# Kernel optimization log

Hardware: AMD Instinct MI355X
Metric: run time of the kernel (lower is better)

## Reference

```python
import jax, jax.numpy as jnp
import numpy as np

L, B, H, HC = 2048, 64, 1024, 1024
NEG = -1e10


def setup_inputs() -> dict:
    key = jax.random.key(0)
    k1, k2, k3, k4, k5, k6 = jax.random.split(key, 6)
    prev_layer_outputs = jax.random.normal(k1, (L, B, H), dtype=jnp.float32)
    hidden = jax.random.normal(k2, (B, H), dtype=jnp.float32)
    mask = jax.random.randint(k3, (B, L), 0, 2, dtype=jnp.int32)
    # learned params: e = Linear(2H -> HC), v = Linear(HC -> 1, no bias)
    s_e = 1.0 / np.sqrt(2 * H)
    W_e = jax.random.uniform(k4, (HC, 2 * H), minval=-s_e, maxval=s_e, dtype=jnp.float32)
    b_e = jax.random.uniform(k5, (HC,), minval=-s_e, maxval=s_e, dtype=jnp.float32)
    s_v = 1.0 / np.sqrt(HC)
    W_v = jax.random.uniform(k6, (HC,), minval=-s_v, maxval=s_v, dtype=jnp.float32)
    return {"prev_layer_outputs": prev_layer_outputs, "hidden": hidden, "mask": mask,
            "W_e": W_e, "b_e": b_e, "W_v": W_v}


def reference(prev_layer_outputs, hidden, mask, W_e, b_e, W_v):
    # prev_layer_outputs: [L, B, H] -> [B, L, H]
    outs = jnp.transpose(prev_layer_outputs, (1, 0, 2))
    # repeat hidden over L and concat on feature dim: [B, L, 2H]
    hid = jnp.broadcast_to(hidden[:, None, :], (outs.shape[0], outs.shape[1], hidden.shape[-1]))
    cat = jnp.concatenate([hid, outs], axis=-1)
    # energy: tanh(Linear(2H -> HC))
    energy = jnp.tanh(jnp.einsum('blf,cf->blc', cat, W_e) + b_e)
    # score: Linear(HC -> 1), squeeze -> [B, L]
    attention = jnp.einsum('blc,c->bl', energy, W_v)
    attention = jnp.where(mask == 0, jnp.float32(NEG), attention)
    attention_weights = jax.nn.softmax(attention, axis=1)  # [B, L]
    # weighted sum over L -> [B, H], then to [1, B, H]
    weighted = jnp.einsum('bl,blh->bh', attention_weights, outs)
    return weighted[None, :, :]
```

## Files before the change

### kernel.cpp

```cpp
#include <hip/hip_runtime.h>
#include <hip/hip_bf16.h>
#include <stdint.h>

#define LDIM 2048
#define BDIM 64
#define HDIM 1024
#define HCDIM 1024
#define CAPROWS 98304

typedef __attribute__((ext_vector_type(8))) short short8;
typedef __attribute__((ext_vector_type(4))) short s16x4;
typedef __attribute__((ext_vector_type(4))) float f32x4;

static __device__ __forceinline__ short f2bf(float f) {
  union { float f; uint32_t u; } a; a.f = f;
  uint32_t r = a.u + 0x7fffu + ((a.u >> 16) & 1u);
  return (short)(r >> 16);
}
static __device__ __forceinline__ float bf2f(short s) {
  union { uint32_t u; float f; } a;
  a.u = ((uint32_t)(unsigned short)s) << 16;
  return a.f;
}
static __device__ __forceinline__ float fast_tanh(float x) {
  x = fminf(15.f, fmaxf(-15.f, x));
  float e = __expf(2.f * x);
  return (e - 1.f) * __builtin_amdgcn_rcpf(e + 1.f);
}

#define GL16(gp, lp) __builtin_amdgcn_global_load_lds(                           \
    (const __attribute__((address_space(1))) void*)(gp),                         \
    (__attribute__((address_space(3))) void*)(lp), 16, 0, 0)

__global__ void scan_mask(const int* __restrict__ mask, int* __restrict__ bases) {
  __shared__ int sc[512];
  const int t = threadIdx.x;
  int cnt = 0;
  #pragma unroll 8
  for (int b = 0; b < 64; ++b) {
    int4 v = *(const int4*)&mask[b * 2048 + t * 4];
    cnt += v.x + v.y + v.z + v.w;
  }
  sc[t] = cnt;
  __syncthreads();
  for (int off = 1; off < 512; off <<= 1) {
    int v = (t >= off) ? sc[t - off] : 0;
    __syncthreads();
    sc[t] += v;
    __syncthreads();
  }
  bases[t] = sc[t] - cnt;
  if (t == 511) bases[512] = sc[511];
}

__global__ void gather_rows(const float* __restrict__ prev, const int* __restrict__ mask,
                            const int* __restrict__ bases, short* __restrict__ A_c,
                            int* __restrict__ cm2m, int* __restrict__ m2cm) {
  __shared__ int smm[256];
  __shared__ int swt[4];
  const int c = blockIdx.x, t = threadIdx.x;
  const int base = bases[c];
  int bit = 0, p = 0, wv = 0;
  if (t < 256) {
    const int m = c * 256 + t;
    bit = (mask[(t & 63) * 2048 + (m >> 6)] != 0);
    unsigned long long bal = __ballot(bit);
    const int lane = t & 63;
    wv = t >> 6;
    p = __popcll(bal & ((1ull << lane) - 1ull));
    if (lane == 0) swt[wv] = (int)__popcll(bal);
  }
  __syncthreads();
  if (t < 256 && bit) {
    int off = p;
    for (int i = 0; i < wv; ++i) off += swt[i];
    const int cm = base + off;
    smm[off] = t;
    if (cm < CAPROWS) {
      cm2m[cm] = c * 256 + t;
      m2cm[c * 256 + t] = cm;
    }
  }
  __syncthreads();
  const int cnt = swt[0] + swt[1] + swt[2] + swt[3];
  const int col = (t & 255) * 4;
  for (int r = (t >> 8); r < cnt; r += 2) {
    const int lm = smm[r];
    const float4 v = *(const float4*)(prev + (((size_t)(c * 256 + lm)) << 10) + col);
    if (base + r < CAPROWS) {
      s16x4 o = { f2bf(v.x), f2bf(v.y), f2bf(v.z), f2bf(v.w) };
      *(s16x4*)&A_c[(((size_t)(base + r)) << 10) + col] = o;
    }
  }
}

__global__ void convert_we(const float* __restrict__ We, short* __restrict__ Wb) {
  int g = blockIdx.x * 256 + threadIdx.x;
  int c = g >> 8;
  int j = (g & 255) * 4;
  float4 v = *(const float4*)(We + (size_t)c * 2048 + 1024 + j);
  s16x4 o = { f2bf(v.x), f2bf(v.y), f2bf(v.z), f2bf(v.w) };
  *(s16x4*)(Wb + (size_t)c * 1024 + j) = o;
}

__global__ void hidbias_kernel(const float* __restrict__ We, const float* __restrict__ hidden,
                               const float* __restrict__ be, float* __restrict__ hidbias) {
  __shared__ float wrow[1024];
  int c0 = blockIdx.x * 16;
  int t = threadIdx.x;
  int b = t >> 2, q = t & 3;
  for (int ci = 0; ci < 16; ++ci) {
    int c = c0 + ci;
    *(float4*)&wrow[t * 4] = *(const float4*)&We[(size_t)c * 2048 + t * 4];
    __syncthreads();
    float s0 = 0.f, s1 = 0.f;
    const float* hb = hidden + b * 1024;
    #pragma unroll 8
    for (int j = 0; j < 256; j += 2) {
      int i0 = q + 4 * j;
      s0 += wrow[i0] * hb[i0];
      s1 += wrow[i0 + 4] * hb[i0 + 4];
    }
    float s = s0 + s1;
    s += __shfl_xor(s, 1);
    s += __shfl_xor(s, 2);
    if (q == 0) hidbias[b * 1024 + c] = s + be[c];
    __syncthreads();
  }
}

__global__ __launch_bounds__(512) void energy_gemm_p6(
    const short* __restrict__ A_c, const short* __restrict__ Wb,
    const float* __restrict__ hidbias, const float* __restrict__ Wv,
    const int* __restrict__ bases, const int* __restrict__ cm2m,
    float* __restrict__ logitsT)
{
  __shared__ short As[4][256][32];
  __shared__ short Bs[4][256][32];
  __shared__ int sidx[256];
  const int Mc0 = bases[512];
  const int Mc = Mc0 < CAPROWS ? Mc0 : CAPROWS;
  const int mt = ((blockIdx.x >> 5) << 3) + (blockIdx.x & 7);
  const int nt = (blockIdx.x >> 3) & 3;
  if (mt * 256 >= Mc) return;
  const int m0 = mt * 256;
  const int n0 = nt * 256;

  const int tid = threadIdx.x;
  const int wave = tid >> 6, lane = tid & 63;
  const int q = lane >> 4, lr = lane & 15;
  const int wr = wave >> 2, wc = wave & 3;

  const int r0 = tid >> 2;
  const int c0s = (((tid & 3) ^ ((r0 >> 1) & 3))) * 8;
  const short* asrc = A_c + (size_t)(m0 + r0) * 1024 + c0s;
  const short* bsrc = Wb  + (size_t)(n0 + r0) * 1024 + c0s;

#define STAGE(buf, ks) do {                                                    \
    const int _ko = (ks) * 32;                                                 \
    GL16(asrc + _ko,          &As[buf][0][0] + tid * 8);                       \
    GL16(asrc + 131072 + _ko, &As[buf][0][0] + tid * 8 + 4096);                \
    GL16(bsrc + _ko,          &Bs[buf][0][0] + tid * 8);                       \
    GL16(bsrc + 131072 + _ko, &Bs[buf][0][0] + tid * 8 + 4096);                \
  } while (0)

  const int crd = (q ^ ((lr >> 1) & 3)) * 8;

#define COMPUTE(buf) do {                                                      \
    short8 af[8], bfr[4];                                                      \
    _Pragma("unroll")                                                          \
    for (int mi = 0; mi < 8; ++mi)                                             \
      af[mi] = *(const short8*)&As[buf][wr * 128 + mi * 16 + lr][crd];         \
    _Pragma("unroll")                                                          \
    for (int ni = 0; ni < 4; ++ni)                                             \
      bfr[ni] = *(const short8*)&Bs[buf][wc * 64 + ni * 16 + lr][crd];         \
    __builtin_amdgcn_s_setprio(1);                                             \
    _Pragma("unroll")                                                          \
    for (int mi = 0; mi < 8; ++mi)                                             \
      _Pragma("unroll")                                                        \
      for (int ni = 0; ni < 4; ++ni)                                           \
        acc[mi][ni] = __builtin_amdgcn_mfma_f32_16x16x32_bf16(                 \
            af[mi], bfr[ni], acc[mi][ni], 0, 0, 0);                            \
    __builtin_amdgcn_s_setprio(0);                                             \
  } while (0)

#define VMW8() asm volatile("s_waitcnt vmcnt(8)" ::: "memory")
#define VMW4() asm volatile("s_waitcnt vmcnt(4)" ::: "memory")
#define VMW0() asm volatile("s_waitcnt vmcnt(0)" ::: "memory")
#define BAR()  asm volatile("s_barrier" ::: "memory")

  f32x4 acc[8][4];
  #pragma unroll
  for (int i = 0; i < 8; ++i)
    #pragma unroll
    for (int j = 0; j < 4; ++j) acc[i][j] = (f32x4){0.f, 0.f, 0.f, 0.f};

  STAGE(0, 0);
  STAGE(1, 1);
  STAGE(2, 2);

  #pragma unroll 4
  for (int ks = 0; ks < 28; ++ks) {
    VMW8(); BAR();
    STAGE((ks + 3) & 3, ks + 3);
    COMPUTE(ks & 3);
  }
  VMW8(); BAR(); STAGE(3, 31); COMPUTE(0);
  VMW8(); BAR(); COMPUTE(1);
  VMW4(); BAR(); COMPUTE(2);
  VMW0(); BAR(); COMPUTE(3);

#undef STAGE
#undef COMPUTE

  if (tid < 256) sidx[tid] = (m0 + tid < Mc) ? cm2m[m0 + tid] : -1;
  __syncthreads();

  float wv[4];
  #pragma unroll
  for (int ni = 0; ni < 4; ++ni) wv[ni] = Wv[n0 + wc * 64 + ni * 16 + lr];

  #pragma unroll
  for (int mi = 0; mi < 8; ++mi) {
    #pragma unroll
    for (int r = 0; r < 4; ++r) {
      const int row = wr * 128 + mi * 16 + 4 * q + r;
      const int mm = sidx[row];
      if (mm >= 0) {
        const int b = mm & 63;
        float s = 0.f;
        #pragma unroll
        for (int ni = 0; ni < 4; ++ni) {
          const int c = n0 + wc * 64 + ni * 16 + lr;
          s += fast_tanh(acc[mi][ni][r] + hidbias[b * 1024 + c]) * wv[ni];
        }
        s += __shfl_xor(s, 1);
        s += __shfl_xor(s, 2);
        s += __shfl_xor(s, 4);
        s += __shfl_xor(s, 8);
        if (lr == 0) atomicAdd(&logitsT[mm], s);
      }
    }
  }
}

__global__ void softstats(const float* __restrict__ logitsT, const int* __restrict__ mask,
                          float* __restrict__ stats) {
  __shared__ float red[8];
  const int b = blockIdx.x, t = threadIdx.x;
  float mx = -1e30f;
  for (int l = t; l < 2048; l += 256)
    if (mask[b * 2048 + l] != 0) mx = fmaxf(mx, logitsT[l * 64 + b]);
  #pragma unroll
  for (int o = 32; o > 0; o >>= 1) mx = fmaxf(mx, __shfl_xor(mx, o));
  if ((t & 63) == 0) red[t >> 6] = mx;
  __syncthreads();
  mx = fmaxf(fmaxf(red[0], red[1]), fmaxf(red[2], red[3]));
  float den = 0.f;
  for (int l = t; l < 2048; l += 256)
    if (mask[b * 2048 + l] != 0) den += __expf(logitsT[l * 64 + b] - mx);
  #pragma unroll
  for (int o = 32; o > 0; o >>= 1) den += __shfl_xor(den, o);
  if ((t & 63) == 0) red[4 + (t >> 6)] = den;
  __syncthreads();
  if (t == 0) {
    stats[b * 2] = mx;
    stats[b * 2 + 1] = 1.f / (red[4] + red[5] + red[6] + red[7]);
  }
}

__global__ void wsum_bf16(const short* __restrict__ A_c, const float* __restrict__ logitsT,
                          const int* __restrict__ mask, const float* __restrict__ stats,
                          const int* __restrict__ m2cm, float* __restrict__ out) {
  const int b = blockIdx.x >> 5;
  const int lc = blockIdx.x & 31;
  const int t = threadIdx.x;
  const float mx = stats[b * 2], invd = stats[b * 2 + 1];
  const int h0 = t * 4;
  float4 a = {0.f, 0.f, 0.f, 0.f};
  for (int l = lc * 64; l < lc * 64 + 64; ++l) {
    if (mask[b * 2048 + l] == 0) continue;
    const unsigned cm = (unsigned)m2cm[l * 64 + b];
    if (cm >= (unsigned)CAPROWS) continue;
    float w = __expf(logitsT[l * 64 + b] - mx) * invd;
    s16x4 v = *(const s16x4*)&A_c[((size_t)cm << 10) + h0];
    a.x += w * bf2f(v.x);
    a.y += w * bf2f(v.y);
    a.z += w * bf2f(v.z);
    a.w += w * bf2f(v.w);
  }
  atomicAdd(&out[b * 1024 + h0 + 0], a.x);
  atomicAdd(&out[b * 1024 + h0 + 1], a.y);
  atomicAdd(&out[b * 1024 + h0 + 2], a.z);
  atomicAdd(&out[b * 1024 + h0 + 3], a.w);
}

extern "C" void kernel_launch(void* const* d_in, const int* in_sizes, int n_in,
                              void* d_out, int out_size, void* d_ws, size_t ws_size,
                              hipStream_t stream) {
  const float* prev   = (const float*)d_in[0];
  const float* hidden = (const float*)d_in[1];
  const int*   mask   = (const int*)d_in[2];
  const float* We     = (const float*)d_in[3];
  const float* be     = (const float*)d_in[4];
  const float* Wv     = (const float*)d_in[5];
  float* out = (float*)d_out;

  char* ws = (char*)d_ws;
  size_t off = 0;
  short* A_c     = (short*)(ws + off); off += (size_t)CAPROWS * 1024 * 2;
  short* Wb      = (short*)(ws + off); off += 2097152;
  float* hidbias = (float*)(ws + off); off += 262144;
  float* logitsT = (float*)(ws + off); off += 524288;
  int*   cm2m    = (int*)  (ws + off); off += (size_t)CAPROWS * 4;
  int*   m2cm    = (int*)  (ws + off); off += 524288;
  int*   bases   = (int*)  (ws + off); off += 4096;
  float* stats   = (float*)(ws + off); off += 1024;

  hipMemsetAsync(d_out, 0, (size_t)out_size * sizeof(float), stream);
  hipMemsetAsync(logitsT, 0, 131072 * sizeof(float), stream);
  scan_mask<<<1, 512, 0, stream>>>(mask, bases);
  gather_rows<<<512, 512, 0, stream>>>(prev, mask, bases, A_c, cm2m, m2cm);
  convert_we<<<1024, 256, 0, stream>>>(We, Wb);
  hidbias_kernel<<<64, 256, 0, stream>>>(We, hidden, be, hidbias);
  energy_gemm_p6<<<2048, 512, 0, stream>>>(A_c, Wb, hidbias, Wv, bases, cm2m, logitsT);
  softstats<<<64, 256, 0, stream>>>(logitsT, mask, stats);
  wsum_bf16<<<2048, 256, 0, stream>>>(A_c, logitsT, mask, stats, m2cm, out);
}
```

Measured before the change: 468.1 us.

## Restructure energy GEMM into 8-phase ping-pong pipeline with 64-wide K tiles

Replaces the 4-buffer, K=32 staging loop with a double-buffered K=64 scheme split into A/B halves. Each K-step is broken into four phases that interleave global-to-LDS loads of the next tile with LDS reads and MFMA batches. Barriers sit between phases and the LDS swizzle changes to an XOR over 8 chunks. The goal is to hide load latency behind matrix math with fewer wait points and bigger tiles. In exchange it adds many more barriers per step, and the last iteration reloads a redundant tile.

```diff
diff --git a/kernel.cpp b/kernel.cpp
--- a/kernel.cpp
+++ b/kernel.cpp
@@ -129,14 +129,14 @@
   }
 }
 
-__global__ __launch_bounds__(512) void energy_gemm_p6(
+__global__ __launch_bounds__(512) void energy_gemm_8p(
     const short* __restrict__ A_c, const short* __restrict__ Wb,
     const float* __restrict__ hidbias, const float* __restrict__ Wv,
     const int* __restrict__ bases, const int* __restrict__ cm2m,
     float* __restrict__ logitsT)
 {
-  __shared__ short As[4][256][32];
-  __shared__ short Bs[4][256][32];
+  __shared__ short Ah[2][2][128][64];
+  __shared__ short Bh[2][2][128][64];
   __shared__ int sidx[256];
   const int Mc0 = bases[512];
   const int Mc = Mc0 < CAPROWS ? Mc0 : CAPROWS;
@@ -150,44 +150,50 @@
   const int wave = tid >> 6, lane = tid & 63;
   const int q = lane >> 4, lr = lane & 15;
   const int wr = wave >> 2, wc = wave & 3;
-
-  const int r0 = tid >> 2;
-  const int c0s = (((tid & 3) ^ ((r0 >> 1) & 3))) * 8;
-  const short* asrc = A_c + (size_t)(m0 + r0) * 1024 + c0s;
-  const short* bsrc = Wb  + (size_t)(n0 + r0) * 1024 + c0s;
-
-#define STAGE(buf, ks) do {                                                    \
-    const int _ko = (ks) * 32;                                                 \
-    GL16(asrc + _ko,          &As[buf][0][0] + tid * 8);                       \
-    GL16(asrc + 131072 + _ko, &As[buf][0][0] + tid * 8 + 4096);                \
-    GL16(bsrc + _ko,          &Bs[buf][0][0] + tid * 8);                       \
-    GL16(bsrc + 131072 + _ko, &Bs[buf][0][0] + tid * 8 + 4096);                \
-  } while (0)
-
-  const int crd = (q ^ ((lr >> 1) & 3)) * 8;
-
-#define COMPUTE(buf) do {                                                      \
-    short8 af[8], bfr[4];                                                      \
+  const int bh = wc >> 1;
+
+  const int sr  = tid >> 3;
+  const int sck = ((tid & 7) ^ ((tid >> 3) & 7)) * 8;
+
+#define STAGE_A(buf, h, kt) do {                                               \
+    const short* _s = A_c + (size_t)(m0 + (h) * 128 + sr) * 1024 + (kt) * 64 + sck; \
+    GL16(_s,         &Ah[buf][h][0][0] + tid * 8);                             \
+    GL16(_s + 65536, &Ah[buf][h][0][0] + tid * 8 + 4096);                      \
+  } while (0)
+#define STAGE_B(buf, h, kt) do {                                               \
+    const short* _s = Wb + (size_t)(n0 + (h) * 128 + sr) * 1024 + (kt) * 64 + sck; \
+    GL16(_s,         &Bh[buf][h][0][0] + tid * 8);                             \
+    GL16(_s + 65536, &Bh[buf][h][0][0] + tid * 8 + 4096);                      \
+  } while (0)
+
+#define DSREAD_A(buf, kk) do {                                                 \
     _Pragma("unroll")                                                          \
     for (int mi = 0; mi < 8; ++mi)                                             \
-      af[mi] = *(const short8*)&As[buf][wr * 128 + mi * 16 + lr][crd];         \
+      afA[mi] = *(const short8*)&Ah[buf][wr][mi * 16 + lr]                     \
+                    [((((kk) * 4 + q)) ^ (lr & 7)) * 8];                       \
+  } while (0)
+#define DSREAD_B(dst, buf, kk, p) do {                                         \
     _Pragma("unroll")                                                          \
-    for (int ni = 0; ni < 4; ++ni)                                             \
-      bfr[ni] = *(const short8*)&Bs[buf][wc * 64 + ni * 16 + lr][crd];         \
+    for (int j = 0; j < 2; ++j)                                                \
+      dst[j] = *(const short8*)&Bh[buf][bh][(wc & 1) * 64 + ((p) * 2 + j) * 16 + lr] \
+                   [((((kk) * 4 + q)) ^ (lr & 7)) * 8];                        \
+  } while (0)
+
+#define MM(p, bf) do {                                                         \
     __builtin_amdgcn_s_setprio(1);                                             \
     _Pragma("unroll")                                                          \
-    for (int mi = 0; mi < 8; ++mi)                                             \
-      _Pragma("unroll")                                                        \
-      for (int ni = 0; ni < 4; ++ni)                                           \
-        acc[mi][ni] = __builtin_amdgcn_mfma_f32_16x16x32_bf16(                 \
-            af[mi], bfr[ni], acc[mi][ni], 0, 0, 0);                            \
+    for (int mi = 0; mi < 8; ++mi) {                                           \
+      acc[mi][(p) * 2]     = __builtin_amdgcn_mfma_f32_16x16x32_bf16(          \
+          afA[mi], bf[0], acc[mi][(p) * 2], 0, 0, 0);                          \
+      acc[mi][(p) * 2 + 1] = __builtin_amdgcn_mfma_f32_16x16x32_bf16(          \
+          afA[mi], bf[1], acc[mi][(p) * 2 + 1], 0, 0, 0);                      \
+    }                                                                          \
     __builtin_amdgcn_s_setprio(0);                                             \
   } while (0)
 
-#define VMW8() asm volatile("s_waitcnt vmcnt(8)" ::: "memory")
-#define VMW4() asm volatile("s_waitcnt vmcnt(4)" ::: "memory")
-#define VMW0() asm volatile("s_waitcnt vmcnt(0)" ::: "memory")
-#define BAR()  asm volatile("s_barrier" ::: "memory")
+#define VM2()  asm volatile("s_waitcnt vmcnt(2)" ::: "memory")
+#define LGKM() asm volatile("s_waitcnt lgkmcnt(0)" ::: "memory")
+#define BARR() asm volatile("s_barrier" ::: "memory")
 
   f32x4 acc[8][4];
   #pragma unroll
@@ -195,23 +201,34 @@
     #pragma unroll
     for (int j = 0; j < 4; ++j) acc[i][j] = (f32x4){0.f, 0.f, 0.f, 0.f};
 
-  STAGE(0, 0);
-  STAGE(1, 1);
-  STAGE(2, 2);
-
-  #pragma unroll 4
-  for (int ks = 0; ks < 28; ++ks) {
-    VMW8(); BAR();
-    STAGE((ks + 3) & 3, ks + 3);
-    COMPUTE(ks & 3);
-  }
-  VMW8(); BAR(); STAGE(3, 31); COMPUTE(0);
-  VMW8(); BAR(); COMPUTE(1);
-  VMW4(); BAR(); COMPUTE(2);
-  VMW0(); BAR(); COMPUTE(3);
-
-#undef STAGE
-#undef COMPUTE
+  short8 afA[8], bfrA[2], bfrB[2];
+
+  STAGE_A(0, 0, 0); STAGE_B(0, 0, 0); STAGE_A(0, 1, 0); STAGE_B(0, 1, 0);
+
+  for (int ks = 0; ks < 16; ++ks) {
+    const int cb = ks & 1, nb = cb ^ 1;
+    const int nx = (ks < 15) ? ks + 1 : 15;
+    STAGE_A(nb, 0, nx);
+    VM2(); BARR();
+    DSREAD_A(cb, 0); DSREAD_B(bfrA, cb, 0, 0);
+    LGKM(); MM(0, bfrA); BARR();
+    DSREAD_B(bfrB, cb, 0, 1);
+    STAGE_B(nb, 0, nx);
+    BARR(); LGKM(); MM(1, bfrB); BARR();
+    DSREAD_A(cb, 1); DSREAD_B(bfrA, cb, 1, 0);
+    STAGE_A(nb, 1, nx);
+    BARR(); LGKM(); MM(0, bfrA); BARR();
+    DSREAD_B(bfrB, cb, 1, 1);
+    STAGE_B(nb, 1, nx);
+    BARR(); LGKM(); MM(1, bfrB); BARR();
+  }
+  asm volatile("s_waitcnt vmcnt(0)" ::: "memory");
+
+#undef STAGE_A
+#undef STAGE_B
+#undef DSREAD_A
+#undef DSREAD_B
+#undef MM
 
   if (tid < 256) sidx[tid] = (m0 + tid < Mc) ? cm2m[m0 + tid] : -1;
   __syncthreads();
@@ -323,7 +340,7 @@
   gather_rows<<<512, 512, 0, stream>>>(prev, mask, bases, A_c, cm2m, m2cm);
   convert_we<<<1024, 256, 0, stream>>>(We, Wb);
   hidbias_kernel<<<64, 256, 0, stream>>>(We, hidden, be, hidbias);
-  energy_gemm_p6<<<2048, 512, 0, stream>>>(A_c, Wb, hidbias, Wv, bases, cm2m, logitsT);
+  energy_gemm_8p<<<2048, 512, 0, stream>>>(A_c, Wb, hidbias, Wv, bases, cm2m, logitsT);
   softstats<<<64, 256, 0, stream>>>(logitsT, mask, stats);
   wsum_bf16<<<2048, 256, 0, stream>>>(A_c, logitsT, mask, stats, m2cm, out);
 }
```

Measured after the change: 489.1 us. +4.5%, slower.

## Replace mask scan with atomic row allocation and shrink GEMM tiles to 128

Applied to the files above, without the earlier changes.

Drops the single-block scan_mask kernel and has each gather block claim its compacted output range with an atomicAdd on a global counter. This removes a serial launch, and the row order now depends on atomic scheduling. The energy GEMM moves from 256x256 tiles with 512 threads to 128x128 tiles with 256 threads and two blocks per CU. The aim is to cut wasted work on the partial last tile and to raise occupancy, at the cost of less operand reuse per tile and more redundant loads.

```diff
diff --git a/kernel.cpp b/kernel.cpp
--- a/kernel.cpp
+++ b/kernel.cpp
@@ -32,34 +32,13 @@
     (const __attribute__((address_space(1))) void*)(gp),                         \
     (__attribute__((address_space(3))) void*)(lp), 16, 0, 0)
 
-__global__ void scan_mask(const int* __restrict__ mask, int* __restrict__ bases) {
-  __shared__ int sc[512];
-  const int t = threadIdx.x;
-  int cnt = 0;
-  #pragma unroll 8
-  for (int b = 0; b < 64; ++b) {
-    int4 v = *(const int4*)&mask[b * 2048 + t * 4];
-    cnt += v.x + v.y + v.z + v.w;
-  }
-  sc[t] = cnt;
-  __syncthreads();
-  for (int off = 1; off < 512; off <<= 1) {
-    int v = (t >= off) ? sc[t - off] : 0;
-    __syncthreads();
-    sc[t] += v;
-    __syncthreads();
-  }
-  bases[t] = sc[t] - cnt;
-  if (t == 511) bases[512] = sc[511];
-}
-
 __global__ void gather_rows(const float* __restrict__ prev, const int* __restrict__ mask,
-                            const int* __restrict__ bases, short* __restrict__ A_c,
+                            int* __restrict__ counter, short* __restrict__ A_c,
                             int* __restrict__ cm2m, int* __restrict__ m2cm) {
   __shared__ int smm[256];
   __shared__ int swt[4];
+  __shared__ int sbase;
   const int c = blockIdx.x, t = threadIdx.x;
-  const int base = bases[c];
   int bit = 0, p = 0, wv = 0;
   if (t < 256) {
     const int m = c * 256 + t;
@@ -71,6 +50,10 @@
     if (lane == 0) swt[wv] = (int)__popcll(bal);
   }
   __syncthreads();
+  const int cnt = swt[0] + swt[1] + swt[2] + swt[3];
+  if (t == 0) sbase = atomicAdd(counter, cnt);
+  __syncthreads();
+  const int base = sbase;
   if (t < 256 && bit) {
     int off = p;
     for (int i = 0; i < wv; ++i) off += swt[i];
@@ -82,7 +65,6 @@
     }
   }
   __syncthreads();
-  const int cnt = swt[0] + swt[1] + swt[2] + swt[3];
   const int col = (t & 255) * 4;
   for (int r = (t >> 8); r < cnt; r += 2) {
     const int lm = smm[r];
@@ -129,27 +111,27 @@
   }
 }
 
-__global__ __launch_bounds__(512) void energy_gemm_p6(
+__global__ __launch_bounds__(256, 2) void energy_gemm_128p(
     const short* __restrict__ A_c, const short* __restrict__ Wb,
     const float* __restrict__ hidbias, const float* __restrict__ Wv,
-    const int* __restrict__ bases, const int* __restrict__ cm2m,
+    const int* __restrict__ counter, const int* __restrict__ cm2m,
     float* __restrict__ logitsT)
 {
-  __shared__ short As[4][256][32];
-  __shared__ short Bs[4][256][32];
-  __shared__ int sidx[256];
-  const int Mc0 = bases[512];
+  __shared__ short As[4][128][32];
+  __shared__ short Bs[4][128][32];
+  __shared__ int sidx[128];
+  const int Mc0 = counter[0];
   const int Mc = Mc0 < CAPROWS ? Mc0 : CAPROWS;
-  const int mt = ((blockIdx.x >> 5) << 3) + (blockIdx.x & 7);
-  const int nt = (blockIdx.x >> 3) & 3;
-  if (mt * 256 >= Mc) return;
-  const int m0 = mt * 256;
-  const int n0 = nt * 256;
+  const int mt = ((blockIdx.x >> 6) << 3) + (blockIdx.x & 7);
+  const int nt = (blockIdx.x >> 3) & 7;
+  if (mt * 128 >= Mc) return;
+  const int m0 = mt * 128;
+  const int n0 = nt * 128;
 
   const int tid = threadIdx.x;
   const int wave = tid >> 6, lane = tid & 63;
   const int q = lane >> 4, lr = lane & 15;
-  const int wr = wave >> 2, wc = wave & 3;
+  const int wr = wave >> 1, wc = wave & 1;
 
   const int r0 = tid >> 2;
   const int c0s = (((tid & 3) ^ ((r0 >> 1) & 3))) * 8;
@@ -158,25 +140,25 @@
 
 #define STAGE(buf, ks) do {                                                    \
     const int _ko = (ks) * 32;                                                 \
-    GL16(asrc + _ko,          &As[buf][0][0] + tid * 8);                       \
-    GL16(asrc + 131072 + _ko, &As[buf][0][0] + tid * 8 + 4096);                \
-    GL16(bsrc + _ko,          &Bs[buf][0][0] + tid * 8);                       \
-    GL16(bsrc + 131072 + _ko, &Bs[buf][0][0] + tid * 8 + 4096);                \
+    GL16(asrc + _ko,         &As[buf][0][0] + tid * 8);                        \
+    GL16(asrc + 65536 + _ko, &As[buf][0][0] + tid * 8 + 2048);                 \
+    GL16(bsrc + _ko,         &Bs[buf][0][0] + tid * 8);                        \
+    GL16(bsrc + 65536 + _ko, &Bs[buf][0][0] + tid * 8 + 2048);                 \
   } while (0)
 
   const int crd = (q ^ ((lr >> 1) & 3)) * 8;
 
 #define COMPUTE(buf) do {                                                      \
-    short8 af[8], bfr[4];                                                      \
+    short8 af[4], bfr[4];                                                      \
     _Pragma("unroll")                                                          \
-    for (int mi = 0; mi < 8; ++mi)                                             \
-      af[mi] = *(const short8*)&As[buf][wr * 128 + mi * 16 + lr][crd];         \
+    for (int mi = 0; mi < 4; ++mi)                                             \
+      af[mi] = *(const short8*)&As[buf][wr * 64 + mi * 16 + lr][crd];          \
     _Pragma("unroll")                                                          \
     for (int ni = 0; ni < 4; ++ni)                                             \
       bfr[ni] = *(const short8*)&Bs[buf][wc * 64 + ni * 16 + lr][crd];         \
     __builtin_amdgcn_s_setprio(1);                                             \
     _Pragma("unroll")                                                          \
-    for (int mi = 0; mi < 8; ++mi)                                             \
+    for (int mi = 0; mi < 4; ++mi)                                             \
       _Pragma("unroll")                                                        \
       for (int ni = 0; ni < 4; ++ni)                                           \
         acc[mi][ni] = __builtin_amdgcn_mfma_f32_16x16x32_bf16(                 \
@@ -189,9 +171,9 @@
 #define VMW0() asm volatile("s_waitcnt vmcnt(0)" ::: "memory")
 #define BAR()  asm volatile("s_barrier" ::: "memory")
 
-  f32x4 acc[8][4];
-  #pragma unroll
-  for (int i = 0; i < 8; ++i)
+  f32x4 acc[4][4];
+  #pragma unroll
+  for (int i = 0; i < 4; ++i)
     #pragma unroll
     for (int j = 0; j < 4; ++j) acc[i][j] = (f32x4){0.f, 0.f, 0.f, 0.f};
 
@@ -213,7 +195,7 @@
 #undef STAGE
 #undef COMPUTE
 
-  if (tid < 256) sidx[tid] = (m0 + tid < Mc) ? cm2m[m0 + tid] : -1;
+  if (tid < 128) sidx[tid] = (m0 + tid < Mc) ? cm2m[m0 + tid] : -1;
   __syncthreads();
 
   float wv[4];
@@ -221,10 +203,10 @@
   for (int ni = 0; ni < 4; ++ni) wv[ni] = Wv[n0 + wc * 64 + ni * 16 + lr];
 
   #pragma unroll
-  for (int mi = 0; mi < 8; ++mi) {
+  for (int mi = 0; mi < 4; ++mi) {
     #pragma unroll
     for (int r = 0; r < 4; ++r) {
-      const int row = wr * 128 + mi * 16 + 4 * q + r;
+      const int row = wr * 64 + mi * 16 + 4 * q + r;
       const int mm = sidx[row];
       if (mm >= 0) {
         const int b = mm & 63;
@@ -312,18 +294,17 @@
   short* Wb      = (short*)(ws + off); off += 2097152;
   float* hidbias = (float*)(ws + off); off += 262144;
   float* logitsT = (float*)(ws + off); off += 524288;
+  int*   counter = (int*)  (ws + off); off += 256;
   int*   cm2m    = (int*)  (ws + off); off += (size_t)CAPROWS * 4;
   int*   m2cm    = (int*)  (ws + off); off += 524288;
-  int*   bases   = (int*)  (ws + off); off += 4096;
   float* stats   = (float*)(ws + off); off += 1024;
 
   hipMemsetAsync(d_out, 0, (size_t)out_size * sizeof(float), stream);
-  hipMemsetAsync(logitsT, 0, 131072 * sizeof(float), stream);
-  scan_mask<<<1, 512, 0, stream>>>(mask, bases);
-  gather_rows<<<512, 512, 0, stream>>>(prev, mask, bases, A_c, cm2m, m2cm);
+  hipMemsetAsync(logitsT, 0, 524288 + 256, stream);
+  gather_rows<<<512, 512, 0, stream>>>(prev, mask, counter, A_c, cm2m, m2cm);
   convert_we<<<1024, 256, 0, stream>>>(We, Wb);
   hidbias_kernel<<<64, 256, 0, stream>>>(We, hidden, be, hidbias);
-  energy_gemm_p6<<<2048, 512, 0, stream>>>(A_c, Wb, hidbias, Wv, bases, cm2m, logitsT);
+  energy_gemm_128p<<<8192, 256, 0, stream>>>(A_c, Wb, hidbias, Wv, counter, cm2m, logitsT);
   softstats<<<64, 256, 0, stream>>>(logitsT, mask, stats);
   wsum_bf16<<<2048, 256, 0, stream>>>(A_c, logitsT, mask, stats, m2cm, out);
 }
```

Result: slower. 524.7 us (+12.1%).

## Load GEMM B operand directly to registers from pre-packed layout; fuse softmax into wsum

Applied to the files above, without the earlier changes.

The energy W matrix is now repacked into an MFMA-fragment-ordered layout, so each wave loads its B fragments straight from global memory into double-buffered registers instead of staging them through LDS. This halves LDS traffic and LDS footprint in the GEMM, which could allow higher occupancy. The cost is more redundant global/L2 reads of B across waves. Separately, the softmax statistics kernel is merged into the weighted-sum kernel, saving one launch. In exchange, each of the 2048 blocks now recomputes the full max and denominator over L for its batch row.

```diff
diff --git a/kernel.cpp b/kernel.cpp
--- a/kernel.cpp
+++ b/kernel.cpp
@@ -94,13 +94,14 @@
   }
 }
 
-__global__ void convert_we(const float* __restrict__ We, short* __restrict__ Wb) {
+__global__ void convert_we_pack(const float* __restrict__ We, short* __restrict__ Wb2) {
   int g = blockIdx.x * 256 + threadIdx.x;
   int c = g >> 8;
   int j = (g & 255) * 4;
   float4 v = *(const float4*)(We + (size_t)c * 2048 + 1024 + j);
   s16x4 o = { f2bf(v.x), f2bf(v.y), f2bf(v.z), f2bf(v.w) };
-  *(s16x4*)(Wb + (size_t)c * 1024 + j) = o;
+  const int off = ((c >> 4) * 32 + (j >> 5)) * 512 + ((c & 15) * 4 + ((j >> 3) & 3)) * 8 + (j & 7);
+  *(s16x4*)(Wb2 + off) = o;
 }
 
 __global__ void hidbias_kernel(const float* __restrict__ We, const float* __restrict__ hidden,
@@ -129,14 +130,13 @@
   }
 }
 
-__global__ __launch_bounds__(512) void energy_gemm_p6(
-    const short* __restrict__ A_c, const short* __restrict__ Wb,
+__global__ __launch_bounds__(512) void energy_gemm_breg(
+    const short* __restrict__ A_c, const short* __restrict__ Wb2,
     const float* __restrict__ hidbias, const float* __restrict__ Wv,
     const int* __restrict__ bases, const int* __restrict__ cm2m,
     float* __restrict__ logitsT)
 {
   __shared__ short As[4][256][32];
-  __shared__ short Bs[4][256][32];
   __shared__ int sidx[256];
   const int Mc0 = bases[512];
   const int Mc = Mc0 < CAPROWS ? Mc0 : CAPROWS;
@@ -154,37 +154,40 @@
   const int r0 = tid >> 2;
   const int c0s = (((tid & 3) ^ ((r0 >> 1) & 3))) * 8;
   const short* asrc = A_c + (size_t)(m0 + r0) * 1024 + c0s;
-  const short* bsrc = Wb  + (size_t)(n0 + r0) * 1024 + c0s;
-
-#define STAGE(buf, ks) do {                                                    \
+
+#define STAGE_A(buf, ks) do {                                                  \
     const int _ko = (ks) * 32;                                                 \
     GL16(asrc + _ko,          &As[buf][0][0] + tid * 8);                       \
     GL16(asrc + 131072 + _ko, &As[buf][0][0] + tid * 8 + 4096);                \
-    GL16(bsrc + _ko,          &Bs[buf][0][0] + tid * 8);                       \
-    GL16(bsrc + 131072 + _ko, &Bs[buf][0][0] + tid * 8 + 4096);                \
   } while (0)
 
+  const int c16b = nt * 16 + wc * 4;
+  const int lane4 = (lr * 4 + q) * 8;
+
+#define BLOAD(dst, ks) do {                                                    \
+    _Pragma("unroll")                                                          \
+    for (int ni = 0; ni < 4; ++ni)                                             \
+      dst[ni] = *(const short8*)(Wb2 + (size_t)((c16b + ni) * 32 + (ks)) * 512 + lane4); \
+  } while (0)
+
   const int crd = (q ^ ((lr >> 1) & 3)) * 8;
 
-#define COMPUTE(buf) do {                                                      \
-    short8 af[8], bfr[4];                                                      \
+#define COMPUTE(buf, BSET) do {                                                \
+    short8 af[8];                                                              \
     _Pragma("unroll")                                                          \
     for (int mi = 0; mi < 8; ++mi)                                             \
       af[mi] = *(const short8*)&As[buf][wr * 128 + mi * 16 + lr][crd];         \
-    _Pragma("unroll")                                                          \
-    for (int ni = 0; ni < 4; ++ni)                                             \
-      bfr[ni] = *(const short8*)&Bs[buf][wc * 64 + ni * 16 + lr][crd];         \
     __builtin_amdgcn_s_setprio(1);                                             \
     _Pragma("unroll")                                                          \
     for (int mi = 0; mi < 8; ++mi)                                             \
       _Pragma("unroll")                                                        \
       for (int ni = 0; ni < 4; ++ni)                                           \
         acc[mi][ni] = __builtin_amdgcn_mfma_f32_16x16x32_bf16(                 \
-            af[mi], bfr[ni], acc[mi][ni], 0, 0, 0);                            \
+            af[mi], BSET[ni], acc[mi][ni], 0, 0, 0);                           \
     __builtin_amdgcn_s_setprio(0);                                             \
   } while (0)
 
-#define VMW8() asm volatile("s_waitcnt vmcnt(8)" ::: "memory")
+#define VMW6() asm volatile("s_waitcnt vmcnt(6)" ::: "memory")
 #define VMW4() asm volatile("s_waitcnt vmcnt(4)" ::: "memory")
 #define VMW0() asm volatile("s_waitcnt vmcnt(0)" ::: "memory")
 #define BAR()  asm volatile("s_barrier" ::: "memory")
@@ -195,22 +198,33 @@
     #pragma unroll
     for (int j = 0; j < 4; ++j) acc[i][j] = (f32x4){0.f, 0.f, 0.f, 0.f};
 
-  STAGE(0, 0);
-  STAGE(1, 1);
-  STAGE(2, 2);
-
-  #pragma unroll 4
-  for (int ks = 0; ks < 28; ++ks) {
-    VMW8(); BAR();
-    STAGE((ks + 3) & 3, ks + 3);
-    COMPUTE(ks & 3);
-  }
-  VMW8(); BAR(); STAGE(3, 31); COMPUTE(0);
-  VMW8(); BAR(); COMPUTE(1);
-  VMW4(); BAR(); COMPUTE(2);
-  VMW0(); BAR(); COMPUTE(3);
-
-#undef STAGE
+  short8 bs0[4], bs1[4];
+
+  STAGE_A(0, 0);
+  STAGE_A(1, 1);
+  BLOAD(bs0, 0);
+  STAGE_A(2, 2);
+
+#define ITER(ks, CUR, NXT) do {                                                \
+    BLOAD(NXT, (ks) + 1);                                                      \
+    VMW6(); BAR();                                                             \
+    STAGE_A(((ks) + 3) & 3, (ks) + 3);                                         \
+    COMPUTE((ks) & 3, CUR);                                                    \
+  } while (0)
+
+  #pragma unroll 2
+  for (int ks = 0; ks < 28; ks += 2) {
+    ITER(ks, bs0, bs1);
+    ITER(ks + 1, bs1, bs0);
+  }
+  ITER(28, bs0, bs1);
+  { BLOAD(bs0, 30); VMW6(); BAR(); COMPUTE(1, bs1); }
+  { BLOAD(bs1, 31); VMW4(); BAR(); COMPUTE(2, bs0); }
+  { VMW0(); BAR(); COMPUTE(3, bs1); }
+
+#undef ITER
+#undef STAGE_A
+#undef BLOAD
 #undef COMPUTE
 
   if (tid < 256) sidx[tid] = (m0 + tid < Mc) ? cm2m[m0 + tid] : -1;
@@ -244,10 +258,14 @@
   }
 }
 
-__global__ void softstats(const float* __restrict__ logitsT, const int* __restrict__ mask,
-                          float* __restrict__ stats) {
+__global__ void softmax_wsum(const short* __restrict__ A_c, const float* __restrict__ logitsT,
+                             const int* __restrict__ mask, const int* __restrict__ m2cm,
+                             float* __restrict__ out) {
   __shared__ float red[8];
-  const int b = blockIdx.x, t = threadIdx.x;
+  const int b = blockIdx.x >> 5;
+  const int lc = blockIdx.x & 31;
+  const int t = threadIdx.x;
+
   float mx = -1e30f;
   for (int l = t; l < 2048; l += 256)
     if (mask[b * 2048 + l] != 0) mx = fmaxf(mx, logitsT[l * 64 + b]);
@@ -263,19 +281,8 @@
   for (int o = 32; o > 0; o >>= 1) den += __shfl_xor(den, o);
   if ((t & 63) == 0) red[4 + (t >> 6)] = den;
   __syncthreads();
-  if (t == 0) {
-    stats[b * 2] = mx;
-    stats[b * 2 + 1] = 1.f / (red[4] + red[5] + red[6] + red[7]);
-  }
-}
-
-__global__ void wsum_bf16(const short* __restrict__ A_c, const float* __restrict__ logitsT,
-                          const int* __restrict__ mask, const float* __restrict__ stats,
-                          const int* __restrict__ m2cm, float* __restrict__ out) {
-  const int b = blockIdx.x >> 5;
-  const int lc = blockIdx.x & 31;
-  const int t = threadIdx.x;
-  const float mx = stats[b * 2], invd = stats[b * 2 + 1];
+  const float invd = 1.f / (red[4] + red[5] + red[6] + red[7]);
+
   const int h0 = t * 4;
   float4 a = {0.f, 0.f, 0.f, 0.f};
   for (int l = lc * 64; l < lc * 64 + 64; ++l) {
@@ -309,21 +316,19 @@
   char* ws = (char*)d_ws;
   size_t off = 0;
   short* A_c     = (short*)(ws + off); off += (size_t)CAPROWS * 1024 * 2;
-  short* Wb      = (short*)(ws + off); off += 2097152;
+  short* Wb2     = (short*)(ws + off); off += 2097152;
   float* hidbias = (float*)(ws + off); off += 262144;
   float* logitsT = (float*)(ws + off); off += 524288;
   int*   cm2m    = (int*)  (ws + off); off += (size_t)CAPROWS * 4;
   int*   m2cm    = (int*)  (ws + off); off += 524288;
   int*   bases   = (int*)  (ws + off); off += 4096;
-  float* stats   = (float*)(ws + off); off += 1024;
 
   hipMemsetAsync(d_out, 0, (size_t)out_size * sizeof(float), stream);
-  hipMemsetAsync(logitsT, 0, 131072 * sizeof(float), stream);
+  hipMemsetAsync(logitsT, 0, 524288, stream);
   scan_mask<<<1, 512, 0, stream>>>(mask, bases);
   gather_rows<<<512, 512, 0, stream>>>(prev, mask, bases, A_c, cm2m, m2cm);
-  convert_we<<<1024, 256, 0, stream>>>(We, Wb);
+  convert_we_pack<<<1024, 256, 0, stream>>>(We, Wb2);
   hidbias_kernel<<<64, 256, 0, stream>>>(We, hidden, be, hidbias);
-  energy_gemm_p6<<<2048, 512, 0, stream>>>(A_c, Wb, hidbias, Wv, bases, cm2m, logitsT);
-  softstats<<<64, 256, 0, stream>>>(logitsT, mask, stats);
-  wsum_bf16<<<2048, 256, 0, stream>>>(A_c, logitsT, mask, stats, m2cm, out);
-}
+  energy_gemm_breg<<<2048, 512, 0, stream>>>(A_c, Wb2, hidbias, Wv, bases, cm2m, logitsT);
+  softmax_wsum<<<2048, 256, 0, stream>>>(A_c, logitsT, mask, m2cm, out);
+}
```

Result: slower. 484.1 us (+3.4%).
